# Performance work log

Hardware: AMD Instinct MI355X
Metric: run time of the kernel (lower is better)

Reference implementation:

```python
import jax, jax.numpy as jnp
import numpy as np

K = 2  # active_experts (top-k)


def setup_inputs() -> dict:
    key = jax.random.key(0)
    ks = jax.random.split(key, 7)
    B, S, D, E = 2, 2048, 1024, 8
    H = 4 * D
    sd = 1.0 / np.sqrt(D)
    sh = 1.0 / np.sqrt(H)
    return {
        "x": jax.random.normal(ks[0], (B, S, D), jnp.float32),
        "Wr": jax.random.normal(ks[1], (D, E), jnp.float32) * sd,
        "br": jax.random.normal(ks[2], (E,), jnp.float32) * sd,
        "W1": jax.random.normal(ks[3], (E, D, H), jnp.float32) * sd,
        "b1": jax.random.normal(ks[4], (E, H), jnp.float32) * sd,
        "W2": jax.random.normal(ks[5], (E, H, D), jnp.float32) * sh,
        "b2": jax.random.normal(ks[6], (E, D), jnp.float32) * sh,
    }


def reference(x, Wr, br, W1, b1, W2, b2):
    E = Wr.shape[-1]
    # Router: top-k gating with softmax over only the selected experts.
    scores = jnp.einsum("bsd,de->bse", x, Wr) + br            # [B,S,E]
    _, topk_idx = jax.lax.top_k(scores, K)                     # [B,S,K]
    indicator = jax.nn.one_hot(topk_idx, E, dtype=scores.dtype).sum(-2)  # [B,S,E] 0/1
    neg_inf = jnp.asarray(-jnp.inf, scores.dtype)
    weights = jax.nn.softmax(jnp.where(indicator > 0, scores, neg_inf), axis=-1)

    # Dense masked expert loop (faithful to the original module's math).
    out = jnp.zeros_like(x)
    for i in range(E):
        xi = x * indicator[..., i:i + 1]                       # masked inputs
        h = jax.nn.relu(jnp.einsum("bsd,dh->bsh", xi, W1[i]) + b1[i])
        yi = jnp.einsum("bsh,hd->bsd", h, W2[i]) + b2[i]
        out = out + yi * weights[..., i:i + 1]
    return out
```

## Files before the change

kernel.cpp:

```cpp
#include <hip/hip_runtime.h>
#include <math.h>

#define T_TOKENS 4096
#define D_DIM    1024
#define E_EXP    8
#define H_DIM    4096
#define NSLOT    8192
#define NSLOTP   (NSLOT + 128)

#define LDSTRIDE 40

typedef __attribute__((ext_vector_type(8))) short   short8;
typedef __attribute__((ext_vector_type(4))) float   floatx4;

__device__ __forceinline__ unsigned short f2bf(float f) {
    unsigned int u = __float_as_uint(f);
    u += 0x7fffu + ((u >> 16) & 1u);
    return (unsigned short)(u >> 16);
}
__device__ __forceinline__ short8 pack8(const float4 a, const float4 b) {
    short8 r;
    r[0] = (short)f2bf(a.x); r[1] = (short)f2bf(a.y);
    r[2] = (short)f2bf(a.z); r[3] = (short)f2bf(a.w);
    r[4] = (short)f2bf(b.x); r[5] = (short)f2bf(b.y);
    r[6] = (short)f2bf(b.z); r[7] = (short)f2bf(b.w);
    return r;
}

typedef __attribute__((address_space(1))) const unsigned int guint;
typedef __attribute__((address_space(3))) unsigned int luint;
__device__ __forceinline__ void gl_lds16(const void* g, void* l) {
    __builtin_amdgcn_global_load_lds((guint*)g, (luint*)l, 16, 0, 0);
}

__global__ __launch_bounds__(256)
void moe_router_kernel(const float* __restrict__ x,
                       const float* __restrict__ Wr,
                       const float* __restrict__ br,
                       const float* __restrict__ b2,
                       float* __restrict__ out,
                       int* __restrict__ counts,
                       int* __restrict__ tok_id,
                       float* __restrict__ tok_w)
{
    const int token = blockIdx.x * 4 + (threadIdx.x >> 6);
    const int lane  = threadIdx.x & 63;

    float s[E_EXP];
#pragma unroll
    for (int e = 0; e < E_EXP; e++) s[e] = 0.0f;

    const float* xrow = x + (size_t)token * D_DIM;
#pragma unroll
    for (int i = 0; i < D_DIM / 64; i++) {
        int d = lane + 64 * i;
        float xv = xrow[d];
        const float4* wr4 = (const float4*)(Wr + (size_t)d * E_EXP);
        float4 w0 = wr4[0], w1 = wr4[1];
        s[0] = fmaf(xv, w0.x, s[0]); s[1] = fmaf(xv, w0.y, s[1]);
        s[2] = fmaf(xv, w0.z, s[2]); s[3] = fmaf(xv, w0.w, s[3]);
        s[4] = fmaf(xv, w1.x, s[4]); s[5] = fmaf(xv, w1.y, s[5]);
        s[6] = fmaf(xv, w1.z, s[6]); s[7] = fmaf(xv, w1.w, s[7]);
    }
#pragma unroll
    for (int off = 32; off >= 1; off >>= 1) {
#pragma unroll
        for (int e = 0; e < E_EXP; e++) s[e] += __shfl_xor(s[e], off, 64);
    }
#pragma unroll
    for (int e = 0; e < E_EXP; e++) s[e] += br[e];

    int e0 = 0; float v0 = s[0];
#pragma unroll
    for (int e = 1; e < E_EXP; e++) if (s[e] > v0) { v0 = s[e]; e0 = e; }
    int e1 = (e0 == 0) ? 1 : 0; float v1 = s[e1];
#pragma unroll
    for (int e = 0; e < E_EXP; e++)
        if (e != e0 && s[e] > v1) { v1 = s[e]; e1 = e; }

    float p1 = __expf(v1 - v0);
    float inv = 1.0f / (1.0f + p1);
    float w0 = inv, w1 = p1 * inv;

    if (lane == 0) {
        int slot0 = atomicAdd(&counts[e0], 1);
        tok_id[e0 * T_TOKENS + slot0] = token;
        tok_w [e0 * T_TOKENS + slot0] = w0;
        int slot1 = atomicAdd(&counts[e1], 1);
        tok_id[e1 * T_TOKENS + slot1] = token;
        tok_w [e1 * T_TOKENS + slot1] = w1;
    }

    float* orow = out + (size_t)token * D_DIM;
    const float* b20 = b2 + (size_t)e0 * D_DIM;
    const float* b21 = b2 + (size_t)e1 * D_DIM;
#pragma unroll
    for (int i = 0; i < D_DIM / 64; i++) {
        int d = lane + 64 * i;
        orow[d] = fmaf(w0, b20[d], w1 * b21[d]);
    }
}

__global__ void moe_scan_kernel(const int* __restrict__ counts,
                                int* __restrict__ offs)
{
    if (threadIdx.x == 0) {
        int a = 0;
#pragma unroll
        for (int e = 0; e < E_EXP; e++) { offs[e] = a; a += counts[e]; }
    }
}


__global__ __launch_bounds__(256)
void moe_xgather_kernel(const float* __restrict__ x,
                        const int* __restrict__ offs,
                        const int* __restrict__ tok_id,
                        unsigned short* __restrict__ Xg)
{
    const int gslot = blockIdx.x * 256 + threadIdx.x;
    int e = 0;
#pragma unroll
    for (int i = 1; i < E_EXP; i++) if (gslot >= offs[i]) e = i;
    const int loc = gslot - offs[e];
    const int token = tok_id[e * T_TOKENS + loc];
    const float* xr = x + (size_t)token * D_DIM;
    const int g0 = blockIdx.y * 16;
#pragma unroll
    for (int g = g0; g < g0 + 16; g++) {
        float4 v0 = *(const float4*)(xr + g * 8);
        float4 v1 = *(const float4*)(xr + g * 8 + 4);
        *(short8*)&Xg[((size_t)g * NSLOTP + gslot) * 8] = pack8(v0, v1);
    }
}

__global__ __launch_bounds__(256)
void moe_wstage_kernel(const float* __restrict__ M,
                       unsigned short* __restrict__ S,
                       int R, int C)
{
    __shared__ unsigned short T[64 * 72];
    const int e = blockIdx.z;
    const float* Me = M + (size_t)e * R * C;
    unsigned short* Se = S + (size_t)e * R * C;
    const int c0 = blockIdx.x * 64, r0 = blockIdx.y * 64;
    const int tid = threadIdx.x;
    const int rl = tid >> 2, cc = (tid & 3) * 16;

    const float* src = Me + (size_t)(r0 + rl) * C + c0 + cc;
#pragma unroll
    for (int j = 0; j < 4; j++) {
        float4 v = *(const float4*)(src + 4 * j);
        T[(cc + 4 * j + 0) * 72 + rl] = f2bf(v.x);
        T[(cc + 4 * j + 1) * 72 + rl] = f2bf(v.y);
        T[(cc + 4 * j + 2) * 72 + rl] = f2bf(v.z);
        T[(cc + 4 * j + 3) * 72 + rl] = f2bf(v.w);
    }
    __syncthreads();
#pragma unroll
    for (int it = 0; it < 2; it++) {
        int cell = tid + 256 * it;
        int c = cell & 63, g = cell >> 6;
        short8 v = *(const short8*)&T[c * 72 + g * 8];
        *(short8*)&Se[(((size_t)(r0 >> 3) + g) * C + c0 + c) * 8] = v;
    }
}

__global__ __launch_bounds__(256, 2)
void moe_ffn1_fast(const unsigned short* __restrict__ Xg,
                   const unsigned short* __restrict__ W1S,
                   const float* __restrict__ b1,
                   const int* __restrict__ counts,
                   const int* __restrict__ offs,
                   const float* __restrict__ tok_w,
                   unsigned short* __restrict__ Hbuf)
{
    const int e   = blockIdx.z;
    const int n_e = counts[e];
    const int m0  = blockIdx.y * 128;
    if (m0 >= n_e) return;
    const int h0  = blockIdx.x * 128;
    const int hb  = offs[e];
    const int tid  = threadIdx.x;
    const int lane = tid & 63;
    const int wave = tid >> 6;
    const int wy = (wave >> 1) * 64, wx = (wave & 1) * 64;
    const int ml = lane & 15, q = lane >> 4;

    __shared__ unsigned short As[8 * 128 * 8];
    __shared__ unsigned short Bs[8 * 128 * 8];
    __shared__ float wts_s[128];
    __shared__ float b1s[128];

    if (tid < 128) {
        int slot = m0 + tid;
        wts_s[tid] = (slot < n_e) ? tok_w[e * T_TOKENS + slot] : 0.0f;
        b1s[tid]   = b1[(size_t)e * H_DIM + h0 + tid];
    }

    floatx4 zero = {0.f, 0.f, 0.f, 0.f};
    floatx4 acc[4][4];
#pragma unroll
    for (int i = 0; i < 4; i++)
#pragma unroll
        for (int j = 0; j < 4; j++) acc[i][j] = zero;

    const unsigned short* Be = W1S + (size_t)e * D_DIM * H_DIM;
    const size_t arow = (size_t)(hb + m0);
    const int cell = ((0 * 4 + wave) * 64) + lane;

    for (int kk8 = 0; kk8 < D_DIM / 8; kk8 += 8) {
#pragma unroll
        for (int t = 0; t < 4; t++) {
            int cbase = (t * 4 + wave) * 64;
            int c = cbase + lane;
            int g = c >> 7, r = c & 127;
            gl_lds16(&Xg[((size_t)(kk8 + g) * NSLOTP + arow + r) * 8], &As[cbase * 8]);
            gl_lds16(&Be[((size_t)(kk8 + g) * H_DIM + h0 + r) * 8],    &Bs[cbase * 8]);
        }
        __syncthreads();
#pragma unroll
        for (int ks = 0; ks < 2; ks++) {
            short8 a[4], b[4];
#pragma unroll
            for (int i = 0; i < 4; i++)
                a[i] = *(const short8*)&As[(((ks * 4 + q) * 128) + wy + i * 16 + ml) * 8];
#pragma unroll
            for (int j = 0; j < 4; j++)
                b[j] = *(const short8*)&Bs[(((ks * 4 + q) * 128) + wx + j * 16 + ml) * 8];
#pragma unroll
            for (int i = 0; i < 4; i++)
#pragma unroll
                for (int j = 0; j < 4; j++)
                    acc[i][j] = __builtin_amdgcn_mfma_f32_16x16x32_bf16(
                                    a[i], b[j], acc[i][j], 0, 0, 0);
        }
        __syncthreads();
    }
    (void)cell;

#pragma unroll
    for (int i = 0; i < 4; i++) {
#pragma unroll
        for (int r = 0; r < 4; r++) {
            int row  = wy + i * 16 + q * 4 + r;
            int slot = m0 + row;
            if (slot < n_e) {
                float w = wts_s[row];
                int gslot = hb + slot;
#pragma unroll
                for (int j = 0; j < 4; j++) {
                    int hcol = h0 + wx + j * 16 + ml;
                    float v = fmaxf(acc[i][j][r] + b1s[wx + j * 16 + ml], 0.0f) * w;
                    Hbuf[((size_t)(hcol >> 3) * NSLOTP + gslot) * 8 + (hcol & 7)] = f2bf(v);
                }
            }
        }
    }
}

__global__ __launch_bounds__(256, 2)
void moe_ffn2_fast(const unsigned short* __restrict__ Hbuf,
                   const unsigned short* __restrict__ W2S,
                   float* __restrict__ out,
                   const int* __restrict__ counts,
                   const int* __restrict__ offs,
                   const int* __restrict__ tok_id)
{
    const int e   = blockIdx.z;
    const int n_e = counts[e];
    const int m0  = blockIdx.y * 128;
    if (m0 >= n_e) return;
    const int d0  = (blockIdx.x & 7) * 128;
    const int kb  = (blockIdx.x >> 3) * (H_DIM / 8 / 2);
    const int hb  = offs[e];
    const int tid  = threadIdx.x;
    const int lane = tid & 63;
    const int wave = tid >> 6;
    const int wy = (wave >> 1) * 64, wx = (wave & 1) * 64;
    const int ml = lane & 15, q = lane >> 4;

    __shared__ unsigned short As[8 * 128 * 8];
    __shared__ unsigned short Bs[8 * 128 * 8];
    __shared__ int ids_s[128];

    if (tid < 128) {
        int slot = m0 + tid;
        ids_s[tid] = (slot < n_e) ? tok_id[e * T_TOKENS + slot] : 0;
    }

    floatx4 zero = {0.f, 0.f, 0.f, 0.f};
    floatx4 acc[4][4];
#pragma unroll
    for (int i = 0; i < 4; i++)
#pragma unroll
        for (int j = 0; j < 4; j++) acc[i][j] = zero;

    const unsigned short* Be = W2S + (size_t)e * H_DIM * D_DIM;
    const size_t arow = (size_t)(hb + m0);

    for (int kk8 = kb; kk8 < kb + H_DIM / 8 / 2; kk8 += 8) {
#pragma unroll
        for (int t = 0; t < 4; t++) {
            int cbase = (t * 4 + wave) * 64;
            int c = cbase + lane;
            int g = c >> 7, r = c & 127;
            gl_lds16(&Hbuf[((size_t)(kk8 + g) * NSLOTP + arow + r) * 8], &As[cbase * 8]);
            gl_lds16(&Be[((size_t)(kk8 + g) * D_DIM + d0 + r) * 8],      &Bs[cbase * 8]);
        }
        __syncthreads();
#pragma unroll
        for (int ks = 0; ks < 2; ks++) {
            short8 a[4], b[4];
#pragma unroll
            for (int i = 0; i < 4; i++)
                a[i] = *(const short8*)&As[(((ks * 4 + q) * 128) + wy + i * 16 + ml) * 8];
#pragma unroll
            for (int j = 0; j < 4; j++)
                b[j] = *(const short8*)&Bs[(((ks * 4 + q) * 128) + wx + j * 16 + ml) * 8];
#pragma unroll
            for (int i = 0; i < 4; i++)
#pragma unroll
                for (int j = 0; j < 4; j++)
                    acc[i][j] = __builtin_amdgcn_mfma_f32_16x16x32_bf16(
                                    a[i], b[j], acc[i][j], 0, 0, 0);
        }
        __syncthreads();
    }

#pragma unroll
    for (int i = 0; i < 4; i++) {
#pragma unroll
        for (int r = 0; r < 4; r++) {
            int row  = wy + i * 16 + q * 4 + r;
            int slot = m0 + row;
            if (slot < n_e) {
                float* orow = out + (size_t)ids_s[row] * D_DIM + d0 + wx;
#pragma unroll
                for (int j = 0; j < 4; j++)
                    atomicAdd(&orow[j * 16 + ml], acc[i][j][r]);
            }
        }
    }
}


__global__ __launch_bounds__(256, 2)
void moe_ffn1_kernel(const float* __restrict__ x,
                     const float* __restrict__ W1,
                     const float* __restrict__ b1,
                     const int* __restrict__ counts,
                     const int* __restrict__ offs,
                     const int* __restrict__ tok_id,
                     const float* __restrict__ tok_w,
                     unsigned short* __restrict__ Hbuf)
{
    const int e   = blockIdx.z;
    const int n_e = counts[e];
    const int m0  = blockIdx.y * 128;
    if (m0 >= n_e) return;
    const int h0  = blockIdx.x * 128;
    const int hb  = offs[e];
    const int tid  = threadIdx.x;
    const int lane = tid & 63;
    const int wave = tid >> 6;
    const int wy = (wave >> 1) * 64;
    const int wx = (wave & 1) * 64;
    const int ml = lane & 15;
    const int q  = lane >> 4;

    __shared__ unsigned short xs[128 * LDSTRIDE];
    __shared__ unsigned short wt[128 * LDSTRIDE];
    __shared__ int   ids_s[128];
    __shared__ float wts_s[128];
    __shared__ float b1s[128];

    if (tid < 128) {
        int slot = m0 + tid;
        ids_s[tid] = (slot < n_e) ? tok_id[e * T_TOKENS + slot] : 0;
        wts_s[tid] = (slot < n_e) ? tok_w[e * T_TOKENS + slot] : 0.0f;
        b1s[tid]   = b1[(size_t)e * H_DIM + h0 + tid];
    }
    __syncthreads();

    floatx4 zero = {0.f, 0.f, 0.f, 0.f};
    floatx4 acc[4][4];
#pragma unroll
    for (int i = 0; i < 4; i++)
#pragma unroll
        for (int j = 0; j < 4; j++) acc[i][j] = zero;

    const float* W1e = W1 + (size_t)e * D_DIM * H_DIM + h0;
    const int xr = tid >> 1;
    const int xc = (tid & 1) * 16;
    const int wc = tid & 31;
    const int wk = tid >> 5;
    const size_t xrow_base = (size_t)ids_s[xr] * D_DIM;

    for (int kk = 0; kk < D_DIM; kk += 32) {
        {
            const float* src = x + xrow_base + kk + xc;
            unsigned short* dst = &xs[xr * LDSTRIDE + xc];
#pragma unroll
            for (int i = 0; i < 4; i++) {
                float4 v = *(const float4*)(src + 4 * i);
                ushort4 o = make_ushort4(f2bf(v.x), f2bf(v.y), f2bf(v.z), f2bf(v.w));
                *(ushort4*)(dst + 4 * i) = o;
            }
        }
#pragma unroll
        for (int it = 0; it < 4; it++) {
            int k = wk + 8 * it;
            const float* src = W1e + (size_t)(kk + k) * H_DIM + wc;
#pragma unroll
            for (int j = 0; j < 4; j++)
                wt[(wc + 32 * j) * LDSTRIDE + k] = f2bf(src[32 * j]);
        }
        __syncthreads();

        short8 a[4], b[4];
#pragma unroll
        for (int i = 0; i < 4; i++)
            a[i] = *(const short8*)&xs[(wy + i * 16 + ml) * LDSTRIDE + q * 8];
#pragma unroll
        for (int j = 0; j < 4; j++)
            b[j] = *(const short8*)&wt[(wx + j * 16 + ml) * LDSTRIDE + q * 8];
#pragma unroll
        for (int i = 0; i < 4; i++)
#pragma unroll
            for (int j = 0; j < 4; j++)
                acc[i][j] = __builtin_amdgcn_mfma_f32_16x16x32_bf16(
                                a[i], b[j], acc[i][j], 0, 0, 0);
        __syncthreads();
    }

#pragma unroll
    for (int i = 0; i < 4; i++) {
#pragma unroll
        for (int r = 0; r < 4; r++) {
            int row  = wy + i * 16 + q * 4 + r;
            int slot = m0 + row;
            if (slot < n_e) {
                float w = wts_s[row];
                size_t base = (size_t)(hb + slot) * H_DIM + h0 + wx;
#pragma unroll
                for (int j = 0; j < 4; j++) {
                    float v = acc[i][j][r] + b1s[wx + j * 16 + ml];
                    v = fmaxf(v, 0.0f) * w;
                    Hbuf[base + j * 16 + ml] = f2bf(v);
                }
            }
        }
    }
}

__global__ __launch_bounds__(256, 2)
void moe_ffn2_kernel(const float* __restrict__ W2,
                     float* __restrict__ out,
                     const int* __restrict__ counts,
                     const int* __restrict__ offs,
                     const int* __restrict__ tok_id,
                     const unsigned short* __restrict__ Hbuf)
{
    const int e   = blockIdx.z;
    const int n_e = counts[e];
    const int m0  = blockIdx.y * 128;
    if (m0 >= n_e) return;
    const int d0  = blockIdx.x * 128;
    const int hb  = offs[e];
    const int tid  = threadIdx.x;
    const int lane = tid & 63;
    const int wave = tid >> 6;
    const int wy = (wave >> 1) * 64;
    const int wx = (wave & 1) * 64;
    const int ml = lane & 15;
    const int q  = lane >> 4;

    __shared__ unsigned short hs[128 * LDSTRIDE];
    __shared__ unsigned short wt[128 * LDSTRIDE];
    __shared__ int ids_s[128];

    if (tid < 128) {
        int slot = m0 + tid;
        ids_s[tid] = (slot < n_e) ? tok_id[e * T_TOKENS + slot] : 0;
    }
    __syncthreads();

    floatx4 zero = {0.f, 0.f, 0.f, 0.f};
    floatx4 acc[4][4];
#pragma unroll
    for (int i = 0; i < 4; i++)
#pragma unroll
        for (int j = 0; j < 4; j++) acc[i][j] = zero;

    const float* W2e = W2 + (size_t)e * H_DIM * D_DIM + d0;
    const int xr = tid >> 1;
    const int xc = (tid & 1) * 16;
    const int wc = tid & 31;
    const int wk = tid >> 5;
    const int hrow = min(hb + m0 + xr, NSLOT - 1);
    const size_t hrow_base = (size_t)hrow * H_DIM;

    for (int kk = 0; kk < H_DIM; kk += 32) {
        {
            const unsigned short* src = Hbuf + hrow_base + kk + xc;
            unsigned short* dst = &hs[xr * LDSTRIDE + xc];
#pragma unroll
            for (int i = 0; i < 4; i++)
                *(ushort4*)(dst + 4 * i) = *(const ushort4*)(src + 4 * i);
        }
#pragma unroll
        for (int it = 0; it < 4; it++) {
            int k = wk + 8 * it;
            const float* src = W2e + (size_t)(kk + k) * D_DIM + wc;
#pragma unroll
            for (int j = 0; j < 4; j++)
                wt[(wc + 32 * j) * LDSTRIDE + k] = f2bf(src[32 * j]);
        }
        __syncthreads();

        short8 a[4], b[4];
#pragma unroll
        for (int i = 0; i < 4; i++)
            a[i] = *(const short8*)&hs[(wy + i * 16 + ml) * LDSTRIDE + q * 8];
#pragma unroll
        for (int j = 0; j < 4; j++)
            b[j] = *(const short8*)&wt[(wx + j * 16 + ml) * LDSTRIDE + q * 8];
#pragma unroll
        for (int i = 0; i < 4; i++)
#pragma unroll
            for (int j = 0; j < 4; j++)
                acc[i][j] = __builtin_amdgcn_mfma_f32_16x16x32_bf16(
                                a[i], b[j], acc[i][j], 0, 0, 0);
        __syncthreads();
    }

#pragma unroll
    for (int i = 0; i < 4; i++) {
#pragma unroll
        for (int r = 0; r < 4; r++) {
            int row  = wy + i * 16 + q * 4 + r;
            int slot = m0 + row;
            if (slot < n_e) {
                float* orow = out + (size_t)ids_s[row] * D_DIM + d0 + wx;
#pragma unroll
                for (int j = 0; j < 4; j++)
                    atomicAdd(&orow[j * 16 + ml], acc[i][j][r]);
            }
        }
    }
}


extern "C" void kernel_launch(void* const* d_in, const int* in_sizes, int n_in,
                              void* d_out, int out_size, void* d_ws, size_t ws_size,
                              hipStream_t stream) {
    const float* x  = (const float*)d_in[0];
    const float* Wr = (const float*)d_in[1];
    const float* br = (const float*)d_in[2];
    const float* W1 = (const float*)d_in[3];
    const float* b1 = (const float*)d_in[4];
    const float* W2 = (const float*)d_in[5];
    const float* b2 = (const float*)d_in[6];
    float* out = (float*)d_out;

    int*   counts = (int*)d_ws;
    int*   offs   = (int*)((char*)d_ws + 64);
    int*   tok_id = (int*)((char*)d_ws + 128);
    float* tok_w  = (float*)((char*)d_ws + 128 + E_EXP * T_TOKENS * 4);

    const size_t OFF_XG  = 1u << 20;
    const size_t SZ_XG   = (size_t)(D_DIM / 8) * NSLOTP * 16;
    const size_t OFF_W   = OFF_XG + SZ_XG;
    const size_t SZ_W    = (size_t)E_EXP * D_DIM * H_DIM * 2;
    const size_t OFF_HB  = OFF_W + SZ_W;
    const size_t SZ_HB   = (size_t)(H_DIM / 8) * NSLOTP * 16;
    const size_t NEED_FAST = OFF_HB + SZ_HB;

    hipMemsetAsync(d_ws, 0, 64, stream);

    moe_router_kernel<<<T_TOKENS / 4, 256, 0, stream>>>(
        x, Wr, br, b2, out, counts, tok_id, tok_w);
    moe_scan_kernel<<<1, 64, 0, stream>>>(counts, offs);

    if (ws_size >= NEED_FAST) {
        unsigned short* Xg   = (unsigned short*)((char*)d_ws + OFF_XG);
        unsigned short* Wsh  = (unsigned short*)((char*)d_ws + OFF_W);
        unsigned short* Hbuf = (unsigned short*)((char*)d_ws + OFF_HB);

        moe_xgather_kernel<<<dim3(NSLOT / 256, 8), 256, 0, stream>>>(
            x, offs, tok_id, Xg);

        moe_wstage_kernel<<<dim3(H_DIM / 64, D_DIM / 64, E_EXP), 256, 0, stream>>>(
            W1, Wsh, D_DIM, H_DIM);

        moe_ffn1_fast<<<dim3(H_DIM / 128, T_TOKENS / 128, E_EXP), 256, 0, stream>>>(
            Xg, Wsh, b1, counts, offs, tok_w, Hbuf);

        moe_wstage_kernel<<<dim3(D_DIM / 64, H_DIM / 64, E_EXP), 256, 0, stream>>>(
            W2, Wsh, H_DIM, D_DIM);

        moe_ffn2_fast<<<dim3(16, T_TOKENS / 128, E_EXP), 256, 0, stream>>>(
            Hbuf, Wsh, out, counts, offs, tok_id);
    } else {
        unsigned short* Hbuf = (unsigned short*)((char*)d_ws + 524288);

        dim3 g1(H_DIM / 128, T_TOKENS / 128, E_EXP);
        moe_ffn1_kernel<<<g1, 256, 0, stream>>>(
            x, W1, b1, counts, offs, tok_id, tok_w, Hbuf);

        dim3 g2(D_DIM / 128, T_TOKENS / 128, E_EXP);
        moe_ffn2_kernel<<<g2, 256, 0, stream>>>(
            W2, out, counts, offs, tok_id, Hbuf);
    }
}
```

Before: 631.3 us.

## Merge staging kernels and launch compact per-expert tile lists for FFN GEMMs

After: 653.9 us. +3.6%, slower.

```diff
diff --git a/kernel.cpp b/kernel.cpp
--- a/kernel.cpp
+++ b/kernel.cpp
@@ -7,6 +7,7 @@
 #define H_DIM    4096
 #define NSLOT    8192
 #define NSLOTP   (NSLOT + 128)
+#define MAXTILE  72
 
 #define LDSTRIDE 40
 
@@ -102,48 +103,32 @@
 }
 
 __global__ void moe_scan_kernel(const int* __restrict__ counts,
-                                int* __restrict__ offs)
+                                int* __restrict__ offs,
+                                int* __restrict__ ntiles,
+                                int* __restrict__ tiles)
 {
     if (threadIdx.x == 0) {
-        int a = 0;
-#pragma unroll
-        for (int e = 0; e < E_EXP; e++) { offs[e] = a; a += counts[e]; }
-    }
-}
-
-
-__global__ __launch_bounds__(256)
-void moe_xgather_kernel(const float* __restrict__ x,
-                        const int* __restrict__ offs,
-                        const int* __restrict__ tok_id,
-                        unsigned short* __restrict__ Xg)
-{
-    const int gslot = blockIdx.x * 256 + threadIdx.x;
-    int e = 0;
-#pragma unroll
-    for (int i = 1; i < E_EXP; i++) if (gslot >= offs[i]) e = i;
-    const int loc = gslot - offs[e];
-    const int token = tok_id[e * T_TOKENS + loc];
-    const float* xr = x + (size_t)token * D_DIM;
-    const int g0 = blockIdx.y * 16;
-#pragma unroll
-    for (int g = g0; g < g0 + 16; g++) {
-        float4 v0 = *(const float4*)(xr + g * 8);
-        float4 v1 = *(const float4*)(xr + g * 8 + 4);
-        *(short8*)&Xg[((size_t)g * NSLOTP + gslot) * 8] = pack8(v0, v1);
-    }
-}
-
-__global__ __launch_bounds__(256)
-void moe_wstage_kernel(const float* __restrict__ M,
-                       unsigned short* __restrict__ S,
-                       int R, int C)
+        int a = 0, nt = 0;
+#pragma unroll
+        for (int e = 0; e < E_EXP; e++) {
+            offs[e] = a;
+            int m = (counts[e] + 127) >> 7;
+            for (int t = 0; t < m; t++) tiles[nt++] = (e << 16) | t;
+            a += counts[e];
+        }
+        *ntiles = nt;
+    }
+}
+
+
+__device__ __forceinline__ void wstage_body(const float* __restrict__ M,
+                                            unsigned short* __restrict__ S,
+                                            int R, int C, int bx, int by, int e)
 {
     __shared__ unsigned short T[64 * 72];
-    const int e = blockIdx.z;
     const float* Me = M + (size_t)e * R * C;
     unsigned short* Se = S + (size_t)e * R * C;
-    const int c0 = blockIdx.x * 64, r0 = blockIdx.y * 64;
+    const int c0 = bx * 64, r0 = by * 64;
     const int tid = threadIdx.x;
     const int rl = tid >> 2, cc = (tid & 3) * 16;
 
@@ -166,19 +151,81 @@
     }
 }
 
-__global__ __launch_bounds__(256, 2)
+__device__ __forceinline__ void xgather_body(const float* __restrict__ x,
+                                             const int* __restrict__ offs,
+                                             const int* __restrict__ tok_id,
+                                             unsigned short* __restrict__ Xg,
+                                             int bx)
+{
+    const int gslot = (bx & 31) * 256 + threadIdx.x;
+    int e = 0;
+#pragma unroll
+    for (int i = 1; i < E_EXP; i++) if (gslot >= offs[i]) e = i;
+    const int loc = gslot - offs[e];
+    const int token = tok_id[e * T_TOKENS + loc];
+    const float* xr = x + (size_t)token * D_DIM;
+    const int g0 = (bx >> 5) * 16;
+#pragma unroll
+    for (int g = g0; g < g0 + 16; g++) {
+        float4 v0 = *(const float4*)(xr + g * 8);
+        float4 v1 = *(const float4*)(xr + g * 8 + 4);
+        *(short8*)&Xg[((size_t)g * NSLOTP + gslot) * 8] = pack8(v0, v1);
+    }
+}
+
+__global__ __launch_bounds__(256)
+void moe_wstage_kernel(const float* __restrict__ M, unsigned short* __restrict__ S,
+                       int R, int C)
+{
+    wstage_body(M, S, R, C, blockIdx.x, blockIdx.y, blockIdx.z);
+}
+
+__global__ __launch_bounds__(256)
+void moe_xgather_kernel(const float* __restrict__ x, const int* __restrict__ offs,
+                        const int* __restrict__ tok_id, unsigned short* __restrict__ Xg)
+{
+    xgather_body(x, offs, tok_id, Xg, blockIdx.y * 32 + blockIdx.x);
+}
+
+__global__ __launch_bounds__(256)
+void moe_stage_all(const float* __restrict__ x,
+                   const float* __restrict__ W1,
+                   const float* __restrict__ W2,
+                   const int* __restrict__ offs,
+                   const int* __restrict__ tok_id,
+                   unsigned short* __restrict__ Xg,
+                   unsigned short* __restrict__ W1S,
+                   unsigned short* __restrict__ W2S)
+{
+    const int bid = blockIdx.x;
+    if (bid < 8192) {
+        wstage_body(W1, W1S, D_DIM, H_DIM, bid & 63, (bid >> 6) & 15, bid >> 10);
+    } else if (bid < 16384) {
+        int id = bid - 8192;
+        wstage_body(W2, W2S, H_DIM, D_DIM, id & 15, (id >> 4) & 63, id >> 10);
+    } else {
+        xgather_body(x, offs, tok_id, Xg, bid - 16384);
+    }
+}
+
+
+__global__ __launch_bounds__(256, 4)
 void moe_ffn1_fast(const unsigned short* __restrict__ Xg,
                    const unsigned short* __restrict__ W1S,
                    const float* __restrict__ b1,
                    const int* __restrict__ counts,
                    const int* __restrict__ offs,
                    const float* __restrict__ tok_w,
+                   const int* __restrict__ ntiles,
+                   const int* __restrict__ tiles,
                    unsigned short* __restrict__ Hbuf)
 {
-    const int e   = blockIdx.z;
+    const int ty = blockIdx.y;
+    if (ty >= *ntiles) return;
+    const int pk  = tiles[ty];
+    const int e   = pk >> 16;
+    const int m0  = (pk & 0xffff) << 7;
     const int n_e = counts[e];
-    const int m0  = blockIdx.y * 128;
-    if (m0 >= n_e) return;
     const int h0  = blockIdx.x * 128;
     const int hb  = offs[e];
     const int tid  = threadIdx.x;
@@ -207,7 +254,6 @@
 
     const unsigned short* Be = W1S + (size_t)e * D_DIM * H_DIM;
     const size_t arow = (size_t)(hb + m0);
-    const int cell = ((0 * 4 + wave) * 64) + lane;
 
     for (int kk8 = 0; kk8 < D_DIM / 8; kk8 += 8) {
 #pragma unroll
@@ -237,7 +283,6 @@
         }
         __syncthreads();
     }
-    (void)cell;
 
 #pragma unroll
     for (int i = 0; i < 4; i++) {
@@ -259,18 +304,22 @@
     }
 }
 
-__global__ __launch_bounds__(256, 2)
+__global__ __launch_bounds__(256, 4)
 void moe_ffn2_fast(const unsigned short* __restrict__ Hbuf,
                    const unsigned short* __restrict__ W2S,
                    float* __restrict__ out,
                    const int* __restrict__ counts,
                    const int* __restrict__ offs,
-                   const int* __restrict__ tok_id)
-{
-    const int e   = blockIdx.z;
+                   const int* __restrict__ tok_id,
+                   const int* __restrict__ ntiles,
+                   const int* __restrict__ tiles)
+{
+    const int ty = blockIdx.y;
+    if (ty >= *ntiles) return;
+    const int pk  = tiles[ty];
+    const int e   = pk >> 16;
+    const int m0  = (pk & 0xffff) << 7;
     const int n_e = counts[e];
-    const int m0  = blockIdx.y * 128;
-    if (m0 >= n_e) return;
     const int d0  = (blockIdx.x & 7) * 128;
     const int kb  = (blockIdx.x >> 3) * (H_DIM / 8 / 2);
     const int hb  = offs[e];
@@ -566,42 +615,56 @@
 
     int*   counts = (int*)d_ws;
     int*   offs   = (int*)((char*)d_ws + 64);
-    int*   tok_id = (int*)((char*)d_ws + 128);
-    float* tok_w  = (float*)((char*)d_ws + 128 + E_EXP * T_TOKENS * 4);
+    int*   ntiles = (int*)((char*)d_ws + 128);
+    int*   tiles  = (int*)((char*)d_ws + 192);
+    int*   tok_id = (int*)((char*)d_ws + 4096);
+    float* tok_w  = (float*)((char*)d_ws + 4096 + E_EXP * T_TOKENS * 4);
 
     const size_t OFF_XG  = 1u << 20;
     const size_t SZ_XG   = (size_t)(D_DIM / 8) * NSLOTP * 16;
-    const size_t OFF_W   = OFF_XG + SZ_XG;
+    const size_t OFF_W1  = OFF_XG + SZ_XG;
     const size_t SZ_W    = (size_t)E_EXP * D_DIM * H_DIM * 2;
-    const size_t OFF_HB  = OFF_W + SZ_W;
     const size_t SZ_HB   = (size_t)(H_DIM / 8) * NSLOTP * 16;
-    const size_t NEED_FAST = OFF_HB + SZ_HB;
+    const size_t OFF_HB_A  = OFF_W1 + SZ_W;
+    const size_t NEED_FAST = OFF_HB_A + SZ_HB;
+    const size_t OFF_W2    = OFF_W1 + SZ_W;
+    const size_t OFF_HB_B  = OFF_W2 + SZ_W;
+    const size_t NEED_BIG  = OFF_HB_B + SZ_HB;
 
     hipMemsetAsync(d_ws, 0, 64, stream);
 
     moe_router_kernel<<<T_TOKENS / 4, 256, 0, stream>>>(
         x, Wr, br, b2, out, counts, tok_id, tok_w);
-    moe_scan_kernel<<<1, 64, 0, stream>>>(counts, offs);
-
-    if (ws_size >= NEED_FAST) {
+    moe_scan_kernel<<<1, 64, 0, stream>>>(counts, offs, ntiles, tiles);
+
+    if (ws_size >= NEED_BIG) {
         unsigned short* Xg   = (unsigned short*)((char*)d_ws + OFF_XG);
-        unsigned short* Wsh  = (unsigned short*)((char*)d_ws + OFF_W);
-        unsigned short* Hbuf = (unsigned short*)((char*)d_ws + OFF_HB);
-
-        moe_xgather_kernel<<<dim3(NSLOT / 256, 8), 256, 0, stream>>>(
-            x, offs, tok_id, Xg);
-
+        unsigned short* W1S  = (unsigned short*)((char*)d_ws + OFF_W1);
+        unsigned short* W2S  = (unsigned short*)((char*)d_ws + OFF_W2);
+        unsigned short* Hbuf = (unsigned short*)((char*)d_ws + OFF_HB_B);
+
+        moe_stage_all<<<16384 + 256, 256, 0, stream>>>(
+            x, W1, W2, offs, tok_id, Xg, W1S, W2S);
+
+        moe_ffn1_fast<<<dim3(H_DIM / 128, MAXTILE), 256, 0, stream>>>(
+            Xg, W1S, b1, counts, offs, tok_w, ntiles, tiles, Hbuf);
+
+        moe_ffn2_fast<<<dim3(16, MAXTILE), 256, 0, stream>>>(
+            Hbuf, W2S, out, counts, offs, tok_id, ntiles, tiles);
+    } else if (ws_size >= NEED_FAST) {
+        unsigned short* Xg   = (unsigned short*)((char*)d_ws + OFF_XG);
+        unsigned short* Wsh  = (unsigned short*)((char*)d_ws + OFF_W1);
+        unsigned short* Hbuf = (unsigned short*)((char*)d_ws + OFF_HB_A);
+
+        moe_xgather_kernel<<<dim3(32, 8), 256, 0, stream>>>(x, offs, tok_id, Xg);
         moe_wstage_kernel<<<dim3(H_DIM / 64, D_DIM / 64, E_EXP), 256, 0, stream>>>(
             W1, Wsh, D_DIM, H_DIM);
-
-        moe_ffn1_fast<<<dim3(H_DIM / 128, T_TOKENS / 128, E_EXP), 256, 0, stream>>>(
-            Xg, Wsh, b1, counts, offs, tok_w, Hbuf);
-
+        moe_ffn1_fast<<<dim3(H_DIM / 128, MAXTILE), 256, 0, stream>>>(
+            Xg, Wsh, b1, counts, offs, tok_w, ntiles, tiles, Hbuf);
         moe_wstage_kernel<<<dim3(D_DIM / 64, H_DIM / 64, E_EXP), 256, 0, stream>>>(
             W2, Wsh, H_DIM, D_DIM);
-
-        moe_ffn2_fast<<<dim3(16, T_TOKENS / 128, E_EXP), 256, 0, stream>>>(
-            Hbuf, Wsh, out, counts, offs, tok_id);
+        moe_ffn2_fast<<<dim3(16, MAXTILE), 256, 0, stream>>>(
+            Hbuf, Wsh, out, counts, offs, tok_id, ntiles, tiles);
     } else {
         unsigned short* Hbuf = (unsigned short*)((char*)d_ws + 524288);
 
```
